# Performance work log

Hardware: AMD Instinct MI355X
Metric: run time of the kernel (lower is better)

## Reference

```python
import jax, jax.numpy as jnp
import numpy as np

D = 768  # n_dim


def setup_inputs() -> dict:
    key = jax.random.key(0)
    ks = jax.random.split(key, 9)
    B, S = 4, 4096
    s = 0.02
    return {
        "x": jax.random.normal(ks[0], (B, S, D), dtype=jnp.float32),
        "Wq": jax.random.normal(ks[1], (D, D), dtype=jnp.float32) * s,
        "bq": jax.random.normal(ks[2], (D,), dtype=jnp.float32) * s,
        "Wk": jax.random.normal(ks[3], (D, D), dtype=jnp.float32) * s,
        "bk": jax.random.normal(ks[4], (D,), dtype=jnp.float32) * s,
        "Wv": jax.random.normal(ks[5], (D, D), dtype=jnp.float32) * s,
        "bv": jax.random.normal(ks[6], (D,), dtype=jnp.float32) * s,
        "Wc": jax.random.normal(ks[7], (D, D), dtype=jnp.float32) * s,
        "bc": jax.random.normal(ks[8], (D,), dtype=jnp.float32) * s,
    }


def reference(x, Wq, bq, Wk, bk, Wv, bv, Wc, bc):
    # Faithful to the source's executed math (its head-reshape and masked_fill
    # results are discarded): single-'head' full-dim attention, NO causal mask,
    # scale = n_dim**-0.5, then a transpose(1,2).reshape element permutation.
    B, S, nd = x.shape
    q = jnp.einsum('bsd,ed->bse', x, Wq) + bq  # nn.Linear: x @ W.T + b
    k = jnp.einsum('bsd,ed->bse', x, Wk) + bk
    v = jnp.einsum('bsd,ed->bse', x, Wv) + bv
    att = jnp.einsum('bqd,bkd->bqk', q, k) * (nd ** -0.5)  # [B,S,S]
    att = jax.nn.softmax(att, axis=-1)  # no mask (bug preserved)
    y = jnp.einsum('bqk,bkd->bqd', att, v)  # [B,S,D]
    y = jnp.transpose(y, (0, 2, 1)).reshape(B, S, nd)  # element permutation (bug preserved)
    return jnp.einsum('bsd,ed->bse', y, Wc) + bc
```

## Files before the change

### kernel.cpp

```cpp
#include <hip/hip_runtime.h>
#include <stdint.h>


typedef __bf16 bf16;
typedef __bf16 bf16x4 __attribute__((ext_vector_type(4)));
typedef __bf16 bf16x8 __attribute__((ext_vector_type(8)));
typedef float f32x4 __attribute__((ext_vector_type(4)));

#define OFF_Q    0L
#define OFF_K    25165824L
#define OFF_VT   50331648L
#define OFF_W    75497472L
#define OFF_B    80216064L
#define OFF_FLAG 80222208L
#define OFF_L    80223232L
#define OFF_ATT  80289792L
#define ATT_B    33554432L
#define SD       3145728L
#define KOFF     12582912L
#define VTOFF    25165824L

#define M_PLAIN  0
#define M_TRANSC 1
#define M_EXPSUM 2
#define M_DIVL   3

__device__ __forceinline__ void glds16(const void* g, void* s) {
  __builtin_amdgcn_global_load_lds((const __attribute__((address_space(1))) void*)g,
                                   (__attribute__((address_space(3))) void*)s, 16, 0, 0);
}

#define SBAR()  do { asm volatile("" ::: "memory"); __builtin_amdgcn_s_barrier(); \
                     asm volatile("" ::: "memory"); } while (0)
#define LGKM0() do { asm volatile("s_waitcnt lgkmcnt(0)" ::: "memory"); \
                     __builtin_amdgcn_sched_barrier(0); } while (0)

#define MFMA2(ac, aa, bb) do { \
  ac = __builtin_amdgcn_mfma_f32_16x16x32_bf16((bb)[0], (aa)[0], ac, 0, 0, 0); \
  ac = __builtin_amdgcn_mfma_f32_16x16x32_bf16((bb)[1], (aa)[1], ac, 0, 0, 0); \
} while (0)
#define MFMA2T(ac, aa, bb) do { \
  ac = __builtin_amdgcn_mfma_f32_16x16x32_bf16((aa)[0], (bb)[0], ac, 0, 0, 0); \
  ac = __builtin_amdgcn_mfma_f32_16x16x32_bf16((aa)[1], (bb)[1], ac, 0, 0, 0); \
} while (0)

#define CLUSTER(I0, JO, AF) do { \
  if (MODE == M_TRANSC) { \
    _Pragma("unroll") for (int i = 0; i < 4; ++i) \
      _Pragma("unroll") for (int j = 0; j < 2; ++j) MFMA2T(acc[(I0)+i][(JO)+j], AF[i], bF[(JO)+j]); \
  } else { \
    _Pragma("unroll") for (int i = 0; i < 4; ++i) \
      _Pragma("unroll") for (int j = 0; j < 2; ++j) MFMA2(acc[(I0)+i][(JO)+j], AF[i], bF[(JO)+j]); \
  } \
} while (0)

__device__ __forceinline__ void norm8(const void* __restrict__ src, bf16* __restrict__ dst,
                                      long i, long n8, int f)
{
  if (i >= n8) return;
  bf16x8 o;
  if (f) {
    const float4 a = ((const float4*)src)[2 * i];
    const float4 b = ((const float4*)src)[2 * i + 1];
    o[0] = (bf16)a.x; o[1] = (bf16)a.y; o[2] = (bf16)a.z; o[3] = (bf16)a.w;
    o[4] = (bf16)b.x; o[5] = (bf16)b.y; o[6] = (bf16)b.z; o[7] = (bf16)b.w;
  } else {
    o = ((const bf16x8*)src)[i];
  }
  ((bf16x8*)dst)[i] = o;
}

__global__ void normalize_all(const void* x,
                              const void* w0, const void* b0, const void* w1, const void* b1,
                              const void* w2, const void* b2, const void* w3, const void* b3,
                              bf16* __restrict__ xn, bf16* __restrict__ Wn,
                              bf16* __restrict__ bn, int* __restrict__ flagOut)
{
  const int t = threadIdx.x;
  __shared__ int sflag;
  if (t == 0) sflag = 0;
  __syncthreads();
  {
    const uint16_t* xu = (const uint16_t*)x;
    const int e = (xu[2 * t] >> 7) & 0xFF;
    if (e >= 0xE0) sflag = 1;
  }
  __syncthreads();
  const int f = sflag;
  int b = blockIdx.x;
  if (b == 0 && t == 0) *flagOut = f;

  if (b < 6144) { norm8(x, xn, (long)b * 256 + t, 1572864L, f); return; }
  b -= 6144;
  if (b < 1152) {
    const int w = b / 288;
    const void* s = (w == 0) ? w0 : (w == 1) ? w1 : (w == 2) ? w2 : w3;
    norm8(s, Wn + (long)w * 589824L, (long)(b % 288) * 256 + t, 73728L, f);
    return;
  }
  b -= 1152;
  const void* s = (b == 0) ? b0 : (b == 1) ? b1 : (b == 2) ? b2 : b3;
  norm8(s, bn + (long)b * 768L, (long)t, 96L, f);
}

template <int MODE>
__launch_bounds__(512, 2)
__global__ void gemm256(const bf16* __restrict__ A, int lda, long strideA,
                        const bf16* __restrict__ Bm, int ldb, long strideB,
                        void* __restrict__ Cv, int ldc, long strideC,
                        int K, const bf16* __restrict__ bias, float alpha,
                        const int* __restrict__ oflag, float* __restrict__ lsum)
{
  __shared__ bf16 lds[65536];
  A  += (long)blockIdx.z * strideA;
  Bm += (long)blockIdx.z * strideB;
  if (MODE == M_EXPSUM || MODE == M_DIVL) lsum += (long)blockIdx.z * 65536L;

  const int gx = gridDim.x, gy = gridDim.y;
  const int lin = blockIdx.y * gx + blockIdx.x;
  const int cpx = (gx * gy) >> 3;
  const int nlin = (lin & 7) * cpx + (lin >> 3);
  const long m0 = (long)(nlin / gx) * 256, n0 = (long)(nlin % gx) * 256;

  const int tid = threadIdx.x;
  const int wv = tid >> 6, lane = tid & 63;
  const int lr = lane & 15, quad = lane >> 4;
  const int wm = (wv >> 2) << 7;
  const int wn = (wv & 3) << 6;

  f32x4 acc[8][4];
  const f32x4 zero = {0.f, 0.f, 0.f, 0.f};
#pragma unroll
  for (int i = 0; i < 8; ++i)
#pragma unroll
    for (int j = 0; j < 4; ++j) acc[i][j] = zero;

  const int rowid = (wv << 4) + (lane >> 3);
  const int colsw = ((lane & 7) ^ ((lane >> 3) & 7)) << 3;
  const long lda8 = 8L * lda, ldb8 = 8L * ldb;
  const bf16* paL = A + (m0 + rowid) * (long)lda + colsw;
  const bf16* paH = paL + 128L * lda;
  const bf16* pbL = Bm + (n0 + rowid) * (long)ldb + colsw;
  const bf16* pbH = pbL + 128L * ldb;

  auto STG = [&](const bf16* src, long ld8, int tbuf, int reg) {
    bf16* d = lds + (tbuf << 15) + (reg << 13) + (wv << 10);
    glds16(src, d);
    glds16(src + ld8, d + 512);
  };

  const int regA = 1 + ((wv >> 2) << 1);
  const int regB = wv & 2;
  const int aoff = lr << 6;
  const int boff = ((wv & 1) << 12) + (lr << 6);
  const int xo  = (lr & 7) << 3;
  const int ok0 = (quad << 3) ^ xo;
  const int ok1 = (32 + (quad << 3)) ^ xo;

  const int nt = K >> 6;

  STG(pbL, ldb8, 0, 0); STG(paL, lda8, 0, 1);
  STG(pbH, ldb8, 0, 2); STG(paH, lda8, 0, 3);
  asm volatile("s_waitcnt vmcnt(4)" ::: "memory");
  STG(pbL + 64, ldb8, 1, 0); STG(paL + 64, lda8, 1, 1);
  STG(pbH + 64, ldb8, 1, 2);
  asm volatile("s_waitcnt vmcnt(6)" ::: "memory");
  SBAR();

  for (int t = 0; t < nt; ++t) {
    const int buf = t & 1;
    const long k64 = (long)t << 6;
    const bf16* LA = lds + (buf << 15) + (regA << 13) + aoff;
    const bf16* LB = lds + (buf << 15) + (regB << 13) + boff;
    bf16x8 aL[4][2], aH[4][2], bF[4][2];

#pragma unroll
    for (int i = 0; i < 4; ++i) {
      aL[i][0] = *(const bf16x8*)(LA + i * 1024 + ok0);
      aL[i][1] = *(const bf16x8*)(LA + i * 1024 + ok1);
    }
#pragma unroll
    for (int j = 0; j < 4; ++j) {
      bF[j][0] = *(const bf16x8*)(LB + j * 1024 + ok0);
      bF[j][1] = *(const bf16x8*)(LB + j * 1024 + ok1);
    }
    if (t + 1 < nt) STG(paH + k64 + 64, lda8, (t + 1) & 1, 3);
    SBAR();
    LGKM0();
    __builtin_amdgcn_s_setprio(1);
    CLUSTER(0, 0, aL);
    __builtin_amdgcn_s_setprio(0);
    SBAR();

#pragma unroll
    for (int i = 0; i < 4; ++i) {
      aH[i][0] = *(const bf16x8*)(LA + (4 + i) * 1024 + ok0);
      aH[i][1] = *(const bf16x8*)(LA + (4 + i) * 1024 + ok1);
    }
    if (t + 2 < nt) STG(pbL + k64 + 128, ldb8, buf, 0);
    SBAR();
    LGKM0();
    __builtin_amdgcn_s_setprio(1);
    CLUSTER(4, 0, aH);
    __builtin_amdgcn_s_setprio(0);
    SBAR();

    if (t + 2 < nt) STG(paL + k64 + 128, lda8, buf, 1);
    SBAR();
    __builtin_amdgcn_s_setprio(1);
    CLUSTER(0, 2, aL);
    __builtin_amdgcn_s_setprio(0);
    SBAR();

    if (t + 2 < nt) STG(pbH + k64 + 128, ldb8, buf, 2);
    SBAR();
    __builtin_amdgcn_s_setprio(1);
    CLUSTER(4, 2, aH);
    __builtin_amdgcn_s_setprio(0);
    if (t + 2 < nt) asm volatile("s_waitcnt vmcnt(6)" ::: "memory");
    else            asm volatile("s_waitcnt vmcnt(0)" ::: "memory");
    SBAR();
  }

  if (MODE == M_TRANSC) {
#pragma unroll
    for (int j = 0; j < 4; ++j) {
      const long col = n0 + wn + j * 16 + lr;
      const float bv = (float)bias[col];
#pragma unroll
      for (int i = 0; i < 8; ++i) {
        const long row = m0 + wm + i * 16 + quad * 4;
        bf16x4 v4;
#pragma unroll
        for (int r = 0; r < 4; ++r) v4[r] = (bf16)((acc[i][j][r] + bv) * alpha);
        *(bf16x4*)((bf16*)Cv + (long)blockIdx.z * strideC + col * (long)ldc + row) = v4;
      }
    }
    return;
  }

  float* fsh = (float*)lds;

  if (MODE == M_DIVL) {
    if (tid < 256) {
      float s = 0.f;
#pragma unroll
      for (int cg = 0; cg < 16; ++cg) s += lsum[cg * 4096 + n0 + tid];
      fsh[tid] = 1.0f / s;
    }
    __syncthreads();
  }

  const int outf32 = (MODE == M_PLAIN) && (oflag != nullptr) && (*oflag != 0);
  long colb[4];
  f32x4 addv[4];
#pragma unroll
  for (int j = 0; j < 4; ++j) {
    colb[j] = n0 + wn + j * 16 + quad * 4;
    if (MODE == M_PLAIN) {
      const bf16x4 bb = *(const bf16x4*)(bias + colb[j]);
#pragma unroll
      for (int r = 0; r < 4; ++r) addv[j][r] = (float)bb[r];
    } else if (MODE == M_DIVL) {
      addv[j] = *(const f32x4*)(fsh + (int)(colb[j] - n0));
    }
  }
#pragma unroll
  for (int i = 0; i < 8; ++i) {
    const long row = m0 + wm + i * 16 + lr;
    char* rowp = (char*)Cv + ((long)blockIdx.z * strideC + row * (long)ldc) * (outf32 ? 4 : 2);
    float rsum = 0.f;
#pragma unroll
    for (int j = 0; j < 4; ++j) {
      f32x4 v;
#pragma unroll
      for (int r = 0; r < 4; ++r) {
        float t = acc[i][j][r];
        if (MODE == M_PLAIN)       t = (t + addv[j][r]) * alpha;
        else if (MODE == M_EXPSUM) t = __expf(t);
        else if (MODE == M_DIVL)   t = t * addv[j][r];
        v[r] = t;
      }
      if (MODE == M_PLAIN && outf32) {
        *(f32x4*)(rowp + colb[j] * 4) = v;
      } else {
        bf16x4 v4;
#pragma unroll
        for (int r = 0; r < 4; ++r) v4[r] = (bf16)v[r];
        if (MODE == M_EXPSUM) {
#pragma unroll
          for (int r = 0; r < 4; ++r) rsum += (float)v4[r];
        }
        *(bf16x4*)(rowp + colb[j] * 2) = v4;
      }
    }
    if (MODE == M_EXPSUM) {
      rsum += __shfl_xor(rsum, 16);
      rsum += __shfl_xor(rsum, 32);
      if (quad == 0) fsh[((wm + i * 16 + lr) << 2) + (wv & 3)] = rsum;
    }
  }
  if (MODE == M_EXPSUM) {
    __syncthreads();
    if (tid < 256) {
      const f32x4 p = *(const f32x4*)(fsh + (tid << 2));
      lsum[(n0 >> 8) * 4096L + m0 + tid] = p[0] + p[1] + p[2] + p[3];
    }
  }
}

extern "C" void kernel_launch(void* const* d_in, const int* in_sizes, int n_in,
                              void* d_out, int out_size, void* d_ws, size_t ws_size,
                              hipStream_t stream)
{
  (void)in_sizes; (void)n_in; (void)out_size;
  char* ws = (char*)d_ws;

  if (ws_size < (size_t)(OFF_ATT + ATT_B)) return;
  const size_t avail = ws_size - (size_t)OFF_ATT;
  int group = (int)(avail / (size_t)ATT_B);
  group = group >= 4 ? 4 : (group >= 2 ? 2 : 1);

  bf16*  q    = (bf16*)(ws + OFF_Q);
  bf16*  k    = (bf16*)(ws + OFF_K);
  bf16*  vT2  = (bf16*)(ws + OFF_VT);
  bf16*  Wn   = (bf16*)(ws + OFF_W);
  bf16*  bn   = (bf16*)(ws + OFF_B);
  int*   flg  = (int*)(ws + OFF_FLAG);
  bf16*  att  = (bf16*)(ws + OFF_ATT);
  bf16*  xn   = att;
  float* lsum2 = (float*)(ws + OFF_W);

  dim3 blk(256, 1, 1), blk2(512, 1, 1);
  const float qs = 0.03608439182435161f;

  normalize_all<<<7300, blk, 0, stream>>>(d_in[0],
                                          d_in[1], d_in[2], d_in[3], d_in[4],
                                          d_in[5], d_in[6], d_in[7], d_in[8],
                                          xn, Wn, bn, flg);

  dim3 gproj(3, 64, 1);
  gemm256<M_PLAIN><<<gproj, blk2, 0, stream>>>(xn, 768, 0, Wn + 0 * 589824L, 768, 0,
                                               q, 768, 0, 768, bn + 0, qs, nullptr, nullptr);
  gemm256<M_PLAIN><<<gproj, blk2, 0, stream>>>(xn, 768, 0, Wn + 1 * 589824L, 768, 0,
                                               k, 768, 0, 768, bn + 768, 1.f, nullptr, nullptr);
  gemm256<M_TRANSC><<<gproj, blk2, 0, stream>>>(xn, 768, 0, Wn + 2 * 589824L, 768, 0,
                                                vT2, 16384, 0, 768, bn + 1536, 1.f, nullptr, nullptr);

  for (int g = 0; g < 4; g += group) {
    dim3 gs(16, 16, group);
    gemm256<M_EXPSUM><<<gs, blk2, 0, stream>>>(q + g * SD, 768, SD, k + g * SD, 768, SD,
                                               att, 4096, 16777216L, 768, nullptr, 1.f,
                                               nullptr, lsum2 + g * 65536L);
    dim3 gpv(16, 3, group);
    gemm256<M_DIVL><<<gpv, blk2, 0, stream>>>(vT2 + g * 4096L, 16384, 4096L,
                                              att, 4096, 16777216L,
                                              q + g * SD, 4096, SD, 4096, nullptr, 1.f,
                                              nullptr, lsum2 + g * 65536L);
  }

  dim3 gout(3, 64, 1);
  gemm256<M_PLAIN><<<gout, blk2, 0, stream>>>(q, 768, 0, Wn + 3 * 589824L, 768, 0,
                                              d_out, 768, 0, 768, bn + 2304, 1.f, flg, nullptr);
}
```

Before: 486.5 us.

## Make QK^T exp-sum GEMM persistent over four N tiles per block

Adds an NT template parameter so each block of the QK^T exp-sum GEMM computes four consecutive 256-wide column tiles, reusing the same A (Q) row tile. The K-loop prefetch runs continuously across tile boundaries, and the epilogue is emitted inline between tiles. This launches 256 blocks instead of 1024, which removes tail effects and per-block prologue cost and keeps the pipeline full. The trade-off is serialized epilogues inside the loop and a fixed, hard-coded tile mapping that assumes this exact shape.

```diff
diff --git a/kernel.cpp b/kernel.cpp
--- a/kernel.cpp
+++ b/kernel.cpp
@@ -103,7 +103,7 @@
   norm8(s, bn + (long)b * 768L, (long)t, 96L, f);
 }
 
-template <int MODE>
+template <int MODE, int NT = 1>
 __launch_bounds__(512, 2)
 __global__ void gemm256(const bf16* __restrict__ A, int lda, long strideA,
                         const bf16* __restrict__ Bm, int ldb, long strideB,
@@ -112,15 +112,26 @@
                         const int* __restrict__ oflag, float* __restrict__ lsum)
 {
   __shared__ bf16 lds[65536];
-  A  += (long)blockIdx.z * strideA;
-  Bm += (long)blockIdx.z * strideB;
-  if (MODE == M_EXPSUM || MODE == M_DIVL) lsum += (long)blockIdx.z * 65536L;
-
-  const int gx = gridDim.x, gy = gridDim.y;
-  const int lin = blockIdx.y * gx + blockIdx.x;
-  const int cpx = (gx * gy) >> 3;
-  const int nlin = (lin & 7) * cpx + (lin >> 3);
-  const long m0 = (long)(nlin / gx) * 256, n0 = (long)(nlin % gx) * 256;
+  __shared__ float fshx[(NT > 1) ? 1024 : 1];
+
+  long m0, n0; int zdec;
+  if constexpr (NT > 1) {
+    const int p = blockIdx.x;
+    zdec = p >> 6;
+    const int qq = p & 63, jj = qq >> 3;
+    m0 = (long)(2 * (qq & 7) + (jj >> 2)) * 256;
+    n0 = (long)((jj & 3) * 4) * 256;
+  } else {
+    zdec = blockIdx.z;
+    const int gx = gridDim.x, gy = gridDim.y;
+    const int lin = blockIdx.y * gx + blockIdx.x;
+    const int cpx = (gx * gy) >> 3;
+    const int nlin = (lin & 7) * cpx + (lin >> 3);
+    m0 = (long)(nlin / gx) * 256; n0 = (long)(nlin % gx) * 256;
+  }
+  A  += (long)zdec * strideA;
+  Bm += (long)zdec * strideB;
+  if (MODE == M_EXPSUM || MODE == M_DIVL) lsum += (long)zdec * 65536L;
 
   const int tid = threadIdx.x;
   const int wv = tid >> 6, lane = tid & 63;
@@ -157,7 +168,97 @@
   const int ok0 = (quad << 3) ^ xo;
   const int ok1 = (32 + (quad << 3)) ^ xo;
 
-  const int nt = K >> 6;
+  const int ntk = K >> 6;
+  const int NU  = NT * ntk;
+  const long nstep = 256L * ldb;
+
+  auto epi = [&](long n0e) {
+    if constexpr (MODE == M_TRANSC) {
+#pragma unroll
+      for (int j = 0; j < 4; ++j) {
+        const long col = n0e + wn + j * 16 + lr;
+        const float bv = (float)bias[col];
+#pragma unroll
+        for (int i = 0; i < 8; ++i) {
+          const long row = m0 + wm + i * 16 + quad * 4;
+          bf16x4 v4;
+#pragma unroll
+          for (int r = 0; r < 4; ++r) v4[r] = (bf16)((acc[i][j][r] + bv) * alpha);
+          *(bf16x4*)((bf16*)Cv + (long)zdec * strideC + col * (long)ldc + row) = v4;
+        }
+      }
+      return;
+    }
+    float* fsh = (NT > 1) ? fshx : (float*)lds;
+
+    if constexpr (MODE == M_DIVL) {
+      if (tid < 256) {
+        float s = 0.f;
+#pragma unroll
+        for (int cg = 0; cg < 16; ++cg) s += lsum[cg * 4096 + n0e + tid];
+        fsh[tid] = 1.0f / s;
+      }
+      __syncthreads();
+    }
+
+    const int outf32 = (MODE == M_PLAIN) && (oflag != nullptr) && (*oflag != 0);
+    long colb[4];
+    f32x4 addv[4];
+#pragma unroll
+    for (int j = 0; j < 4; ++j) {
+      colb[j] = n0e + wn + j * 16 + quad * 4;
+      if (MODE == M_PLAIN) {
+        const bf16x4 bb = *(const bf16x4*)(bias + colb[j]);
+#pragma unroll
+        for (int r = 0; r < 4; ++r) addv[j][r] = (float)bb[r];
+      } else if (MODE == M_DIVL) {
+        addv[j] = *(const f32x4*)(fsh + (int)(colb[j] - n0e));
+      }
+    }
+#pragma unroll
+    for (int i = 0; i < 8; ++i) {
+      const long row = m0 + wm + i * 16 + lr;
+      char* rowp = (char*)Cv + ((long)zdec * strideC + row * (long)ldc) * (outf32 ? 4 : 2);
+      float rsum = 0.f;
+#pragma unroll
+      for (int j = 0; j < 4; ++j) {
+        f32x4 v;
+#pragma unroll
+        for (int r = 0; r < 4; ++r) {
+          float t = acc[i][j][r];
+          if (MODE == M_PLAIN)       t = (t + addv[j][r]) * alpha;
+          else if (MODE == M_EXPSUM) t = __expf(t);
+          else if (MODE == M_DIVL)   t = t * addv[j][r];
+          v[r] = t;
+        }
+        if (MODE == M_PLAIN && outf32) {
+          *(f32x4*)(rowp + colb[j] * 4) = v;
+        } else {
+          bf16x4 v4;
+#pragma unroll
+          for (int r = 0; r < 4; ++r) v4[r] = (bf16)v[r];
+          if (MODE == M_EXPSUM) {
+#pragma unroll
+            for (int r = 0; r < 4; ++r) rsum += (float)v4[r];
+          }
+          *(bf16x4*)(rowp + colb[j] * 2) = v4;
+        }
+      }
+      if (MODE == M_EXPSUM) {
+        rsum += __shfl_xor(rsum, 16);
+        rsum += __shfl_xor(rsum, 32);
+        if (quad == 0) fsh[((wm + i * 16 + lr) << 2) + (wv & 3)] = rsum;
+      }
+    }
+    if (MODE == M_EXPSUM) {
+      asm volatile("s_waitcnt lgkmcnt(0)" ::: "memory");
+      __builtin_amdgcn_s_barrier();
+      if (tid < 256) {
+        const f32x4 pp = *(const f32x4*)(fsh + (tid << 2));
+        lsum[(n0e >> 8) * 4096L + m0 + tid] = pp[0] + pp[1] + pp[2] + pp[3];
+      }
+    }
+  };
 
   STG(pbL, ldb8, 0, 0); STG(paL, lda8, 0, 1);
   STG(pbH, ldb8, 0, 2); STG(paH, lda8, 0, 3);
@@ -167,9 +268,18 @@
   asm volatile("s_waitcnt vmcnt(6)" ::: "memory");
   SBAR();
 
-  for (int t = 0; t < nt; ++t) {
-    const int buf = t & 1;
-    const long k64 = (long)t << 6;
+  int kt = 0;
+  long boB = 0;
+  long n0t = n0;
+  for (int u = 0; u < NU; ++u) {
+    const int buf = u & 1;
+    int ka3 = kt + 1; if (ka3 == ntk) ka3 = 0;
+    int kt2 = kt + 2; long bt2 = boB;
+    if (kt2 >= ntk) { kt2 -= ntk; bt2 += nstep; }
+    const long ao3 = (long)ka3 << 6;
+    const long ao2 = (long)kt2 << 6;
+    const long bo2 = bt2 + ((long)kt2 << 6);
+
     const bf16* LA = lds + (buf << 15) + (regA << 13) + aoff;
     const bf16* LB = lds + (buf << 15) + (regB << 13) + boff;
     bf16x8 aL[4][2], aH[4][2], bF[4][2];
@@ -184,7 +294,7 @@
       bF[j][0] = *(const bf16x8*)(LB + j * 1024 + ok0);
       bF[j][1] = *(const bf16x8*)(LB + j * 1024 + ok1);
     }
-    if (t + 1 < nt) STG(paH + k64 + 64, lda8, (t + 1) & 1, 3);
+    if (u + 1 < NU) STG(paH + ao3, lda8, (u + 1) & 1, 3);
     SBAR();
     LGKM0();
     __builtin_amdgcn_s_setprio(1);
@@ -197,7 +307,7 @@
       aH[i][0] = *(const bf16x8*)(LA + (4 + i) * 1024 + ok0);
       aH[i][1] = *(const bf16x8*)(LA + (4 + i) * 1024 + ok1);
     }
-    if (t + 2 < nt) STG(pbL + k64 + 128, ldb8, buf, 0);
+    if (u + 2 < NU) STG(pbL + bo2, ldb8, buf, 0);
     SBAR();
     LGKM0();
     __builtin_amdgcn_s_setprio(1);
@@ -205,108 +315,37 @@
     __builtin_amdgcn_s_setprio(0);
     SBAR();
 
-    if (t + 2 < nt) STG(paL + k64 + 128, lda8, buf, 1);
+    if (u + 2 < NU) STG(paL + ao2, lda8, buf, 1);
     SBAR();
     __builtin_amdgcn_s_setprio(1);
     CLUSTER(0, 2, aL);
     __builtin_amdgcn_s_setprio(0);
     SBAR();
 
-    if (t + 2 < nt) STG(pbH + k64 + 128, ldb8, buf, 2);
+    if (u + 2 < NU) STG(pbH + bo2, ldb8, buf, 2);
     SBAR();
     __builtin_amdgcn_s_setprio(1);
     CLUSTER(4, 2, aH);
     __builtin_amdgcn_s_setprio(0);
-    if (t + 2 < nt) asm volatile("s_waitcnt vmcnt(6)" ::: "memory");
+    if (u + 2 < NU) asm volatile("s_waitcnt vmcnt(6)" ::: "memory");
     else            asm volatile("s_waitcnt vmcnt(0)" ::: "memory");
     SBAR();
-  }
-
-  if (MODE == M_TRANSC) {
-#pragma unroll
-    for (int j = 0; j < 4; ++j) {
-      const long col = n0 + wn + j * 16 + lr;
-      const float bv = (float)bias[col];
-#pragma unroll
-      for (int i = 0; i < 8; ++i) {
-        const long row = m0 + wm + i * 16 + quad * 4;
-        bf16x4 v4;
-#pragma unroll
-        for (int r = 0; r < 4; ++r) v4[r] = (bf16)((acc[i][j][r] + bv) * alpha);
-        *(bf16x4*)((bf16*)Cv + (long)blockIdx.z * strideC + col * (long)ldc + row) = v4;
-      }
-    }
-    return;
-  }
-
-  float* fsh = (float*)lds;
-
-  if (MODE == M_DIVL) {
-    if (tid < 256) {
-      float s = 0.f;
-#pragma unroll
-      for (int cg = 0; cg < 16; ++cg) s += lsum[cg * 4096 + n0 + tid];
-      fsh[tid] = 1.0f / s;
-    }
-    __syncthreads();
-  }
-
-  const int outf32 = (MODE == M_PLAIN) && (oflag != nullptr) && (*oflag != 0);
-  long colb[4];
-  f32x4 addv[4];
-#pragma unroll
-  for (int j = 0; j < 4; ++j) {
-    colb[j] = n0 + wn + j * 16 + quad * 4;
-    if (MODE == M_PLAIN) {
-      const bf16x4 bb = *(const bf16x4*)(bias + colb[j]);
-#pragma unroll
-      for (int r = 0; r < 4; ++r) addv[j][r] = (float)bb[r];
-    } else if (MODE == M_DIVL) {
-      addv[j] = *(const f32x4*)(fsh + (int)(colb[j] - n0));
-    }
-  }
-#pragma unroll
-  for (int i = 0; i < 8; ++i) {
-    const long row = m0 + wm + i * 16 + lr;
-    char* rowp = (char*)Cv + ((long)blockIdx.z * strideC + row * (long)ldc) * (outf32 ? 4 : 2);
-    float rsum = 0.f;
-#pragma unroll
-    for (int j = 0; j < 4; ++j) {
-      f32x4 v;
-#pragma unroll
-      for (int r = 0; r < 4; ++r) {
-        float t = acc[i][j][r];
-        if (MODE == M_PLAIN)       t = (t + addv[j][r]) * alpha;
-        else if (MODE == M_EXPSUM) t = __expf(t);
-        else if (MODE == M_DIVL)   t = t * addv[j][r];
-        v[r] = t;
-      }
-      if (MODE == M_PLAIN && outf32) {
-        *(f32x4*)(rowp + colb[j] * 4) = v;
-      } else {
-        bf16x4 v4;
-#pragma unroll
-        for (int r = 0; r < 4; ++r) v4[r] = (bf16)v[r];
-        if (MODE == M_EXPSUM) {
-#pragma unroll
-          for (int r = 0; r < 4; ++r) rsum += (float)v4[r];
-        }
-        *(bf16x4*)(rowp + colb[j] * 2) = v4;
-      }
-    }
-    if (MODE == M_EXPSUM) {
-      rsum += __shfl_xor(rsum, 16);
-      rsum += __shfl_xor(rsum, 32);
-      if (quad == 0) fsh[((wm + i * 16 + lr) << 2) + (wv & 3)] = rsum;
-    }
-  }
-  if (MODE == M_EXPSUM) {
-    __syncthreads();
-    if (tid < 256) {
-      const f32x4 p = *(const f32x4*)(fsh + (tid << 2));
-      lsum[(n0 >> 8) * 4096L + m0 + tid] = p[0] + p[1] + p[2] + p[3];
-    }
-  }
+
+    ++kt;
+    if constexpr (NT > 1) {
+      if (kt == ntk) {
+        kt = 0; boB += nstep;
+        epi(n0t);
+        n0t += 256;
+#pragma unroll
+        for (int i = 0; i < 8; ++i)
+#pragma unroll
+          for (int j = 0; j < 4; ++j) acc[i][j] = zero;
+      }
+    }
+  }
+
+  if constexpr (NT == 1) epi(n0);
 }
 
 extern "C" void kernel_launch(void* const* d_in, const int* in_sizes, int n_in,
@@ -347,16 +386,27 @@
   gemm256<M_TRANSC><<<gproj, blk2, 0, stream>>>(xn, 768, 0, Wn + 2 * 589824L, 768, 0,
                                                 vT2, 16384, 0, 768, bn + 1536, 1.f, nullptr, nullptr);
 
-  for (int g = 0; g < 4; g += group) {
-    dim3 gs(16, 16, group);
-    gemm256<M_EXPSUM><<<gs, blk2, 0, stream>>>(q + g * SD, 768, SD, k + g * SD, 768, SD,
-                                               att, 4096, 16777216L, 768, nullptr, 1.f,
-                                               nullptr, lsum2 + g * 65536L);
-    dim3 gpv(16, 3, group);
-    gemm256<M_DIVL><<<gpv, blk2, 0, stream>>>(vT2 + g * 4096L, 16384, 4096L,
+  if (group == 4) {
+    gemm256<M_EXPSUM, 4><<<dim3(256, 1, 1), blk2, 0, stream>>>(
+        q, 768, SD, k, 768, SD, att, 4096, 16777216L, 768, nullptr, 1.f,
+        nullptr, lsum2);
+    dim3 gpv(16, 3, 4);
+    gemm256<M_DIVL><<<gpv, blk2, 0, stream>>>(vT2, 16384, 4096L,
                                               att, 4096, 16777216L,
-                                              q + g * SD, 4096, SD, 4096, nullptr, 1.f,
-                                              nullptr, lsum2 + g * 65536L);
+                                              q, 4096, SD, 4096, nullptr, 1.f,
+                                              nullptr, lsum2);
+  } else {
+    for (int g = 0; g < 4; g += group) {
+      dim3 gs(16, 16, group);
+      gemm256<M_EXPSUM><<<gs, blk2, 0, stream>>>(q + g * SD, 768, SD, k + g * SD, 768, SD,
+                                                 att, 4096, 16777216L, 768, nullptr, 1.f,
+                                                 nullptr, lsum2 + g * 65536L);
+      dim3 gpv(16, 3, group);
+      gemm256<M_DIVL><<<gpv, blk2, 0, stream>>>(vT2 + g * 4096L, 16384, 4096L,
+                                                att, 4096, 16777216L,
+                                                q + g * SD, 4096, SD, 4096, nullptr, 1.f,
+                                                nullptr, lsum2 + g * 65536L);
+    }
   }
 
   dim3 gout(3, 64, 1);
```

New measurement: 487.3 us. No clear change (+0.1%).

## Add dedicated 64-row PV kernel with register double-buffering for full-batch path

Applied to the files above, without the earlier changes.

When the workspace holds all four batches, the P·V product now goes through a new kernel instead of the generic 256-tile GEMM. Each block handles 64 query rows across all 768 output dims, loading operands straight from global memory into registers with a two-stage prefetch and no LDS staging. It launches 256 blocks, which matches the CU count, where the old path used a 16x3x4 grid. The cost is that every block rereads the full V for its batch with no shared-memory reuse, so the kernel leans more on cache bandwidth.

```diff
diff --git a/kernel.cpp b/kernel.cpp
--- a/kernel.cpp
+++ b/kernel.cpp
@@ -309,6 +309,94 @@
   }
 }
 
+__launch_bounds__(512, 2)
+__global__ void pv64(const bf16* __restrict__ P, const bf16* __restrict__ vt,
+                     bf16* __restrict__ yT, const float* __restrict__ lsum)
+{
+  __shared__ float linv_s[64];
+  const int bid = blockIdx.x;
+  const int x = bid & 7, ii = bid >> 3;
+  const int z = x >> 1;
+  const int qb = ((x & 1) << 5) + ii;
+  const long q0 = (long)qb << 6;
+  const int tid = threadIdx.x;
+  const int wv = tid >> 6, lane = tid & 63;
+  const int lr = lane & 15, quad = lane >> 4;
+
+  if (tid < 64) {
+    const float* lp = lsum + (long)z * 65536L + q0 + tid;
+    float s = 0.f;
+#pragma unroll
+    for (int cg = 0; cg < 16; ++cg) s += lp[cg * 4096];
+    linv_s[tid] = 1.0f / s;
+  }
+  __syncthreads();
+
+  const bf16* Pb = P + (long)z * 16777216L + q0 * 4096L;
+  const bf16* Vb = vt + (long)z * 4096L;
+
+  const bf16* pA[4];
+  const bf16* vA[6];
+#pragma unroll
+  for (int i = 0; i < 4; ++i) pA[i] = Pb + (long)(16 * i + lr) * 4096L + quad * 8;
+#pragma unroll
+  for (int j = 0; j < 6; ++j) vA[j] = Vb + (long)(96 * wv + 16 * j + lr) * 16384L + quad * 8;
+
+  f32x4 acc[4][6];
+  const f32x4 zero = {0.f, 0.f, 0.f, 0.f};
+#pragma unroll
+  for (int i = 0; i < 4; ++i)
+#pragma unroll
+    for (int j = 0; j < 6; ++j) acc[i][j] = zero;
+
+  bf16x8 fa[4], fv[6], fa2[4], fv2[6];
+#pragma unroll
+  for (int i = 0; i < 4; ++i) fa[i] = *(const bf16x8*)(pA[i]);
+#pragma unroll
+  for (int j = 0; j < 6; ++j) fv[j] = *(const bf16x8*)(vA[j]);
+
+  for (int kk = 0; kk < 128; kk += 2) {
+    const long o1 = (long)(kk + 1) * 32;
+#pragma unroll
+    for (int i = 0; i < 4; ++i) fa2[i] = *(const bf16x8*)(pA[i] + o1);
+#pragma unroll
+    for (int j = 0; j < 6; ++j) fv2[j] = *(const bf16x8*)(vA[j] + o1);
+#pragma unroll
+    for (int i = 0; i < 4; ++i)
+#pragma unroll
+      for (int j = 0; j < 6; ++j)
+        acc[i][j] = __builtin_amdgcn_mfma_f32_16x16x32_bf16(fa[i], fv[j], acc[i][j], 0, 0, 0);
+    if (kk + 2 < 128) {
+      const long o2 = (long)(kk + 2) * 32;
+#pragma unroll
+      for (int i = 0; i < 4; ++i) fa[i] = *(const bf16x8*)(pA[i] + o2);
+#pragma unroll
+      for (int j = 0; j < 6; ++j) fv[j] = *(const bf16x8*)(vA[j] + o2);
+    }
+#pragma unroll
+    for (int i = 0; i < 4; ++i)
+#pragma unroll
+      for (int j = 0; j < 6; ++j)
+        acc[i][j] = __builtin_amdgcn_mfma_f32_16x16x32_bf16(fa2[i], fv2[j], acc[i][j], 0, 0, 0);
+  }
+
+  f32x4 lv[4];
+#pragma unroll
+  for (int i = 0; i < 4; ++i) lv[i] = *(const f32x4*)(linv_s + 16 * i + quad * 4);
+#pragma unroll
+  for (int j = 0; j < 6; ++j) {
+    const long d = 96 * wv + 16 * j + lr;
+    bf16* rowp = yT + (long)z * SD + d * 4096L + q0;
+#pragma unroll
+    for (int i = 0; i < 4; ++i) {
+      bf16x4 v4;
+#pragma unroll
+      for (int r = 0; r < 4; ++r) v4[r] = (bf16)(acc[i][j][r] * lv[i][r]);
+      *(bf16x4*)(rowp + 16 * i + quad * 4) = v4;
+    }
+  }
+}
+
 extern "C" void kernel_launch(void* const* d_in, const int* in_sizes, int n_in,
                               void* d_out, int out_size, void* d_ws, size_t ws_size,
                               hipStream_t stream)
@@ -347,16 +435,24 @@
   gemm256<M_TRANSC><<<gproj, blk2, 0, stream>>>(xn, 768, 0, Wn + 2 * 589824L, 768, 0,
                                                 vT2, 16384, 0, 768, bn + 1536, 1.f, nullptr, nullptr);
 
-  for (int g = 0; g < 4; g += group) {
-    dim3 gs(16, 16, group);
-    gemm256<M_EXPSUM><<<gs, blk2, 0, stream>>>(q + g * SD, 768, SD, k + g * SD, 768, SD,
+  if (group == 4) {
+    dim3 gs(16, 16, 4);
+    gemm256<M_EXPSUM><<<gs, blk2, 0, stream>>>(q, 768, SD, k, 768, SD,
                                                att, 4096, 16777216L, 768, nullptr, 1.f,
-                                               nullptr, lsum2 + g * 65536L);
-    dim3 gpv(16, 3, group);
-    gemm256<M_DIVL><<<gpv, blk2, 0, stream>>>(vT2 + g * 4096L, 16384, 4096L,
-                                              att, 4096, 16777216L,
-                                              q + g * SD, 4096, SD, 4096, nullptr, 1.f,
-                                              nullptr, lsum2 + g * 65536L);
+                                               nullptr, lsum2);
+    pv64<<<dim3(256, 1, 1), blk2, 0, stream>>>(att, vT2, q, lsum2);
+  } else {
+    for (int g = 0; g < 4; g += group) {
+      dim3 gs(16, 16, group);
+      gemm256<M_EXPSUM><<<gs, blk2, 0, stream>>>(q + g * SD, 768, SD, k + g * SD, 768, SD,
+                                                 att, 4096, 16777216L, 768, nullptr, 1.f,
+                                                 nullptr, lsum2 + g * 65536L);
+      dim3 gpv(16, 3, group);
+      gemm256<M_DIVL><<<gpv, blk2, 0, stream>>>(vT2 + g * 4096L, 16384, 4096L,
+                                                att, 4096, 16777216L,
+                                                q + g * SD, 4096, SD, 4096, nullptr, 1.f,
+                                                nullptr, lsum2 + g * 65536L);
+    }
   }
 
   dim3 gout(3, 64, 1);
```

Result: slower. 656.1 us (+34.9%).
